# Kernel optimization log

Measured on AMD Instinct MI355X. Metric: run time of the kernel, lower is better.

The kernel has to match this reference:

```python
import jax, jax.numpy as jnp
import numpy as np

N_NODES = 100000
N_EDGES = 1600000
F_IN, F1, F2, F3 = 128, 128, 128, 64


def setup_inputs() -> dict:
    key = jax.random.key(0)
    ks = jax.random.split(key, 10)
    edge_index = jax.random.randint(ks[0], (2, N_EDGES), 0, N_NODES, dtype=jnp.int64)
    x = jax.random.normal(ks[1], (N_NODES, F_IN), dtype=jnp.float32)
    def glorot(k, fi, fo):
        s = (6.0 / (fi + fo)) ** 0.5
        return jax.random.uniform(k, (fi, fo), jnp.float32, -s, s)
    return {
        "edge_index": edge_index,
        "x": x,
        "W1": glorot(ks[2], F_IN, F1), "b1": jnp.zeros((F1,), jnp.float32),
        "W2": glorot(ks[3], F1, F2), "b2": jnp.zeros((F2,), jnp.float32),
        "W3": glorot(ks[4], F2, F3), "b3": jnp.zeros((F3,), jnp.float32),
        "W_att": glorot(ks[5], F3, F3),
    }


def _gcn_conv(x, W, b, src, dst, deg_inv_sqrt):
    h = x @ W  # [N, Fo]
    norm = deg_inv_sqrt[src] * deg_inv_sqrt[dst]  # [E]
    agg = jax.ops.segment_sum(h[src] * norm[:, None], dst, num_segments=x.shape[0])
    agg = agg + h * (deg_inv_sqrt * deg_inv_sqrt)[:, None]  # self-loop term
    return agg + b


def _attention_pool(emb, W_att):
    # SimGNN attention pooling
    ctx = jnp.tanh(jnp.mean(emb @ W_att, axis=0))          # [F3]
    scores = jax.nn.sigmoid(emb @ ctx)                      # [N]
    return emb.T @ scores[:, None]                          # [F3, 1]


def reference(edge_index, x, W1, b1, W2, b2, W3, b3, W_att):
    src, dst = edge_index[0], edge_index[1]
    n = x.shape[0]
    deg = jax.ops.segment_sum(jnp.ones_like(src, dtype=x.dtype), dst, num_segments=n) + 1.0
    dis = jax.lax.rsqrt(deg)
    h = jax.nn.relu(_gcn_conv(x, W1, b1, src, dst, dis))
    h = jax.nn.relu(_gcn_conv(h, W2, b2, src, dst, dis))
    h = _gcn_conv(h, W3, b3, src, dst, dis)                 # abstract_features [N, F3]
    pooled = _attention_pool(h, W_att)                      # [F3, 1]
    return h, pooled
```

## Files before the change

### kernel.cpp

```cpp
#include <hip/hip_runtime.h>
#include <hip/hip_bf16.h>

#define NN 100000
#define NE 1600000
#define NR 100032
#define NB2 196
#define NBLK 391
#define EPB 4096

#if defined(__has_builtin)
#  if __has_builtin(__builtin_amdgcn_cvt_pk_f32_fp8) && \
      __has_builtin(__builtin_amdgcn_cvt_pk_fp8_f32) && \
      __has_builtin(__builtin_amdgcn_cvt_f32_fp8)
#    define HWF8 1
#  endif
#endif

typedef float f32x2 __attribute__((ext_vector_type(2)));
typedef float f32x4 __attribute__((ext_vector_type(4)));
typedef short bf16x8 __attribute__((ext_vector_type(8)));

static __device__ __forceinline__ float bf2f(__hip_bfloat16 v) { return __bfloat162float(v); }
static __device__ __forceinline__ float bfu(unsigned short w) {
    return __uint_as_float((unsigned)w << 16);
}

static __device__ __forceinline__ float f8d_sw(unsigned b) {
    unsigned e = (b >> 3) & 15u, m = b & 7u;
    float mag;
    if (e == 0) mag = (float)m * 0.001953125f;
    else        mag = __uint_as_float(((e + 120u) << 23) | (m << 20));
    return (b & 0x80u) ? -mag : mag;
}
static __device__ __forceinline__ unsigned char f8e_sw(float x) {
    unsigned u = __float_as_uint(x);
    unsigned s = (u >> 31) << 7;
    unsigned au = u & 0x7fffffffu;
    if (au >= 0x43E00000u) return (unsigned char)(s | 0x7Eu);
    if (au <  0x3A800000u) return (unsigned char)s;
    if (au <  0x3C800000u) {
        float a = __uint_as_float(au);
        int m = (int)rintf(a * 512.0f);
        if (m >= 8) return (unsigned char)(s | 0x08u);
        return (unsigned char)(s | (unsigned)m);
    }
    au += 0x80000u;
    if (au >= 0x43E00000u) return (unsigned char)(s | 0x7Eu);
    unsigned e = (au >> 23) - 120u;
    unsigned m = (au >> 20) & 7u;
    return (unsigned char)(s | (e << 3) | m);
}

static __device__ __forceinline__ float f8d1(unsigned b) {
#ifdef HWF8
    return __builtin_amdgcn_cvt_f32_fp8((int)b, 0);
#else
    return f8d_sw(b);
#endif
}
static __device__ __forceinline__ void f8d2(unsigned short v, float& x0, float& x1) {
#ifdef HWF8
    f32x2 r = __builtin_amdgcn_cvt_pk_f32_fp8((int)(unsigned)v, false);
    x0 = r.x; x1 = r.y;
#else
    x0 = f8d_sw(v & 255u); x1 = f8d_sw(v >> 8);
#endif
}
static __device__ __forceinline__ void f8d4(unsigned u, float* o) {
#ifdef HWF8
    f32x2 lo = __builtin_amdgcn_cvt_pk_f32_fp8((int)u, false);
    f32x2 hi = __builtin_amdgcn_cvt_pk_f32_fp8((int)u, true);
    o[0] = lo.x; o[1] = lo.y; o[2] = hi.x; o[3] = hi.y;
#else
    o[0] = f8d_sw(u & 255u); o[1] = f8d_sw((u >> 8) & 255u);
    o[2] = f8d_sw((u >> 16) & 255u); o[3] = f8d_sw(u >> 24);
#endif
}
static __device__ __forceinline__ unsigned short f8e2(float a, float b) {
#ifdef HWF8
    float ca = fminf(fmaxf(a, -448.0f), 448.0f);
    float cb = fminf(fmaxf(b, -448.0f), 448.0f);
    int p = __builtin_amdgcn_cvt_pk_fp8_f32(ca, cb, 0, false);
    return (unsigned short)(p & 0xFFFF);
#else
    return (unsigned short)f8e_sw(a) | ((unsigned short)f8e_sw(b) << 8);
#endif
}
static __device__ __forceinline__ unsigned char f8e1(float a) {
    return (unsigned char)(f8e2(a, 0.0f) & 0xFF);
}
static __device__ __forceinline__ unsigned bfpack(float lo, float hi) {
    return (__float_as_uint(lo) >> 16) | (__float_as_uint(hi) & 0xFFFF0000u);
}

static __device__ __forceinline__ void acc8_add(f32x2* acc, uint2 v) {
#ifdef HWF8
    acc[0] += __builtin_amdgcn_cvt_pk_f32_fp8((int)v.x, false);
    acc[1] += __builtin_amdgcn_cvt_pk_f32_fp8((int)v.x, true);
    acc[2] += __builtin_amdgcn_cvt_pk_f32_fp8((int)v.y, false);
    acc[3] += __builtin_amdgcn_cvt_pk_f32_fp8((int)v.y, true);
#else
    unsigned u[2] = {v.x, v.y};
#pragma unroll
    for (int q = 0; q < 2; q++) {
        float o[4]; f8d4(u[q], o);
        acc[2 * q]     += (f32x2){o[0], o[1]};
        acc[2 * q + 1] += (f32x2){o[2], o[3]};
    }
#endif
}

__global__ void k_probe1(const unsigned short* __restrict__ xw,
                         const int* __restrict__ ei, int* __restrict__ raw) {
    int i = blockIdx.x * 256 + threadIdx.x;
    int nan = ((xw[i] & 0x7F80u) == 0x7F80u) ? 1 : 0;
    int odd = (ei[2 * i + 1] != 0) ? 1 : 0;
    unsigned long long bn = __ballot(nan);
    unsigned long long bo = __ballot(odd);
    if ((threadIdx.x & 63) == 0) {
        if (bn) atomicAdd(&raw[0], __popcll(bn));
        if (bo) atomicAdd(&raw[1], __popcll(bo));
    }
}
__global__ void k_probe2(const int* __restrict__ raw, int* __restrict__ flags) {
    if (threadIdx.x == 0) {
        flags[0] = (raw[0] > 0) ? 1 : 0;
        flags[1] = (raw[1] == 0) ? 1 : 0;
    }
}

static __device__ __forceinline__ int e_src(const int* ei, int e, int f64) {
    int v = f64 ? ei[2 * e] : ei[e];
    return min(max(v, 0), NN - 1);
}
static __device__ __forceinline__ int e_dst(const int* ei, int e, int f64) {
    int v = f64 ? ei[2 * (NE + e)] : ei[NE + e];
    return min(max(v, 0), NN - 1);
}
static __device__ __forceinline__ float ldx(const void* p, long long i, int f32) {
    return f32 ? ((const float*)p)[i] : bf2f(((const __hip_bfloat16*)p)[i]);
}

__global__ void cvt_params(const void* W1, const void* b1, const void* W2, const void* b2,
                           const void* W3, const void* b3, const void* Wa,
                           unsigned short* W1b, unsigned short* W2b, unsigned short* W3b,
                           float* b1f, float* b2f, float* b3f, float* Waf,
                           const int* flags) {
    int i = blockIdx.x * blockDim.x + threadIdx.x;
    int f = flags[0];
    if (i < 16384) {
        int j = i & 7, l = (i >> 3) & 63, c = (i >> 9) & 7, kc = i >> 12;
        int k = kc * 32 + ((l >> 4)) * 8 + j;
        int col = c * 16 + (l & 15);
        W1b[i] = __bfloat16_as_ushort(__float2bfloat16(ldx(W1, k * 128 + col, f)));
        W2b[i] = __bfloat16_as_ushort(__float2bfloat16(ldx(W2, k * 128 + col, f)));
    }
    if (i < 8192) {
        int j = i & 7, l = (i >> 3) & 63, c = (i >> 9) & 3, kc = i >> 11;
        int k = kc * 32 + ((l >> 4)) * 8 + j;
        int col = c * 16 + (l & 15);
        W3b[i] = __bfloat16_as_ushort(__float2bfloat16(ldx(W3, k * 64 + col, f)));
    }
    if (i < 4096)  Waf[i] = ldx(Wa, i, f);
    if (i < 128)   { b1f[i] = ldx(b1, i, f); b2f[i] = ldx(b2, i, f); }
    if (i < 64)    b3f[i] = ldx(b3, i, f);
}

__global__ void k_cvtx(const void* __restrict__ x, unsigned char* __restrict__ P,
                       const int* __restrict__ flags) {
    int i = blockIdx.x * blockDim.x + threadIdx.x;
    if (i >= (NN * 128) / 4) return;
    unsigned pk;
    if (flags[0]) {
        float4 v = ((const float4*)x)[i];
        pk = (unsigned)f8e2(v.x, v.y) | ((unsigned)f8e2(v.z, v.w) << 16);
    } else {
        ushort4 v = ((const ushort4*)x)[i];
        pk = (unsigned)f8e2(bfu(v.x), bfu(v.y)) | ((unsigned)f8e2(bfu(v.z), bfu(v.w)) << 16);
    }
    ((unsigned*)P)[i] = pk;
}

__global__ __launch_bounds__(256) void k_hist(const int* __restrict__ ei,
                                              int* __restrict__ ghist,
                                              const int* __restrict__ flags) {
    __shared__ int h[NB2];
    int blk = blockIdx.x, t = threadIdx.x;
    for (int i = t; i < NB2; i += 256) h[i] = 0;
    __syncthreads();
    int f64 = flags[1];
    int e0 = blk * EPB;
    for (int i = t; i < EPB; i += 256) {
        int e = e0 + i;
        if (e < NE) atomicAdd(&h[e_dst(ei, e, f64) >> 9], 1);
    }
    __syncthreads();
    for (int i = t; i < NB2; i += 256) ghist[blk * NB2 + i] = h[i];
}

__global__ __launch_bounds__(256) void k_off(const int* __restrict__ ghist,
                                             int* __restrict__ cbase,
                                             int* __restrict__ offm,
                                             int* __restrict__ rowptr) {
    __shared__ int tot[NB2];
    int t = threadIdx.x;
    if (t < NB2) {
        int s = 0;
        for (int blk = 0; blk < NBLK; blk++) s += ghist[blk * NB2 + t];
        tot[t] = s;
    }
    __syncthreads();
    if (t == 0) {
        int run = 0;
        for (int b = 0; b < NB2; b++) { cbase[b] = run; run += tot[b]; }
        cbase[NB2] = run;
        rowptr[NN] = run;
    }
    __syncthreads();
    if (t < NB2) {
        int run = cbase[t];
        for (int blk = 0; blk < NBLK; blk++) {
            offm[blk * NB2 + t] = run;
            run += ghist[blk * NB2 + t];
        }
    }
}

__global__ __launch_bounds__(256) void k_scatter(const int* __restrict__ ei,
                                                 const int* __restrict__ offm,
                                                 int* __restrict__ scratch,
                                                 const int* __restrict__ flags) {
    __shared__ int cur[NB2];
    int blk = blockIdx.x, t = threadIdx.x;
    for (int i = t; i < NB2; i += 256) cur[i] = offm[blk * NB2 + i];
    __syncthreads();
    int f64 = flags[1];
    int e0 = blk * EPB;
    for (int i = t; i < EPB; i += 256) {
        int e = e0 + i;
        if (e < NE) {
            int d = e_dst(ei, e, f64);
            int s = e_src(ei, e, f64);
            int p = atomicAdd(&cur[d >> 9], 1);
            p = min(max(p, 0), NE - 1);
            scratch[p] = s | ((d & 511) << 17);
        }
    }
}

__global__ __launch_bounds__(256) void k_build(const int* __restrict__ scratch,
                                               const int* __restrict__ cbase,
                                               int* __restrict__ rowptr,
                                               float* __restrict__ dis,
                                               int* __restrict__ csr) {
    __shared__ int hist[512];
    __shared__ int base[512];
    __shared__ int sd[256];
    int b = blockIdx.x, t = threadIdx.x;
    int n0 = b << 9;
    int s0 = cbase[b], s1 = cbase[b + 1];
    hist[t] = 0; hist[t + 256] = 0;
    __syncthreads();
    for (int i = s0 + t; i < s1; i += 256) {
        int dlo = (scratch[i] >> 17) & 511;
        atomicAdd(&hist[dlo], 1);
    }
    __syncthreads();
    int v0 = hist[2 * t], v1 = hist[2 * t + 1];
    int s = v0 + v1;
    sd[t] = s; __syncthreads();
    for (int o = 1; o < 256; o <<= 1) {
        int add = (t >= o) ? sd[t - o] : 0;
        __syncthreads();
        sd[t] += add;
        __syncthreads();
    }
    int run = s0 + sd[t] - s;
    base[2 * t] = run;
    base[2 * t + 1] = run + v0;
    int n = n0 + 2 * t;
    if (n < NN) {
        rowptr[n] = run;
        dis[n] = rsqrtf((float)v0 + 1.0f);
    }
    if (n + 1 < NN) {
        rowptr[n + 1] = run + v0;
        dis[n + 1] = rsqrtf((float)v1 + 1.0f);
    }
    __syncthreads();
    for (int i = s0 + t; i < s1; i += 256) {
        int v = scratch[i];
        int dlo = (v >> 17) & 511;
        int p = atomicAdd(&base[dlo], 1);
        p = min(max(p, 0), NE - 1);
        csr[p] = v & 0x1FFFF;
    }
}

template <int NCT>
__global__ __launch_bounds__(256) void k_xf_mfma(const unsigned char* __restrict__ A,
                                                 const unsigned short* __restrict__ Wf,
                                                 const float* __restrict__ dis,
                                                 unsigned char* __restrict__ O) {
    __shared__ unsigned short wl[NCT * 4 * 64 * 8];
    int t = threadIdx.x;
    int n0 = blockIdx.x * 64;
    {
        const uint4* wg = (const uint4*)Wf;
        uint4* wld = (uint4*)wl;
#pragma unroll
        for (int i = 0; i < NCT; i++) wld[i * 256 + t] = wg[i * 256 + t];
    }
    __syncthreads();
    int w = t >> 6, l = t & 63;
    int quad = l >> 4, m = l & 15;
    int arow = n0 + w * 16 + m;
    const unsigned char* ap = A + (size_t)arow * 128 + quad * 8;
    f32x4 acc[NCT];
#pragma unroll
    for (int c = 0; c < NCT; c++) acc[c] = (f32x4){0.0f, 0.0f, 0.0f, 0.0f};
#pragma unroll
    for (int kc = 0; kc < 4; kc++) {
        uint2 g = *(const uint2*)(ap + kc * 32);
        float o[8];
        f8d4(g.x, o); f8d4(g.y, o + 4);
        union { unsigned u[4]; bf16x8 v; } fr;
        fr.u[0] = bfpack(o[0], o[1]);
        fr.u[1] = bfpack(o[2], o[3]);
        fr.u[2] = bfpack(o[4], o[5]);
        fr.u[3] = bfpack(o[6], o[7]);
#pragma unroll
        for (int c = 0; c < NCT; c++) {
            bf16x8 bw = *(const bf16x8*)&wl[((kc * NCT + c) * 64 + l) * 8];
            acc[c] = __builtin_amdgcn_mfma_f32_16x16x32_bf16(fr.v, bw, acc[c], 0, 0, 0);
        }
    }
    int orow0 = n0 + w * 16 + quad * 4;
    float dsc[4];
#pragma unroll
    for (int r = 0; r < 4; r++) {
        int row = orow0 + r;
        dsc[r] = (row < NN) ? dis[row] : 0.0f;
    }
#pragma unroll
    for (int c = 0; c < NCT; c++) {
        int col = c * 16 + m;
#pragma unroll
        for (int r = 0; r < 4; r++) {
            int row = orow0 + r;
            if (row <= NN) O[(size_t)row * (NCT * 16) + col] = f8e1(acc[c][r] * dsc[r]);
        }
    }
}

template <bool RELU>
__global__ __launch_bounds__(256) void k_agg128(const unsigned char* __restrict__ Tb,
                                                const int* __restrict__ rowptr,
                                                const int* __restrict__ csr,
                                                const float* __restrict__ dis,
                                                const float* __restrict__ bias,
                                                unsigned char* __restrict__ H) {
    int n = blockIdx.x * 4 + (threadIdx.x >> 6);
    int lane = threadIdx.x & 63;
    int r = lane >> 4;
    int f = lane & 15;
    int fo = f << 3;
    float dn = dis[n];
    int s0 = rowptr[n], s1 = rowptr[n + 1];
    s0 = min(max(s0, 0), NE); s1 = min(max(s1, s0), NE);
    f32x2 acc[4];
#pragma unroll
    for (int k = 0; k < 4; k++) acc[k] = (f32x2){0.0f, 0.0f};
    if (r == 0) {
        uint2 v = *(const uint2*)(Tb + (((unsigned)n << 7) + (unsigned)fo));
        acc8_add(acc, v);
    }
    for (int base = s0; base < s1; base += 64) {
        int m = min(64, s1 - base);
        unsigned voff = (unsigned)NN << 7;
        if (lane < m) voff = (unsigned)csr[base + lane] << 7;
        int nq = (m + 15) >> 4;
        for (int q = 0; q < nq; q++) {
            int a0 = q * 64 + r * 4;
            unsigned vo0 = (unsigned)__builtin_amdgcn_ds_bpermute(a0,      (int)voff);
            unsigned vo1 = (unsigned)__builtin_amdgcn_ds_bpermute(a0 + 16, (int)voff);
            unsigned vo2 = (unsigned)__builtin_amdgcn_ds_bpermute(a0 + 32, (int)voff);
            unsigned vo3 = (unsigned)__builtin_amdgcn_ds_bpermute(a0 + 48, (int)voff);
            uint2 v0 = *(const uint2*)(Tb + (vo0 + (unsigned)fo));
            uint2 v1 = *(const uint2*)(Tb + (vo1 + (unsigned)fo));
            uint2 v2 = *(const uint2*)(Tb + (vo2 + (unsigned)fo));
            uint2 v3 = *(const uint2*)(Tb + (vo3 + (unsigned)fo));
            acc8_add(acc, v0);
            acc8_add(acc, v1);
            acc8_add(acc, v2);
            acc8_add(acc, v3);
        }
    }
#pragma unroll
    for (int k = 0; k < 4; k++) {
        acc[k].x += __shfl_xor(acc[k].x, 16, 64);
        acc[k].y += __shfl_xor(acc[k].y, 16, 64);
        acc[k].x += __shfl_xor(acc[k].x, 32, 64);
        acc[k].y += __shfl_xor(acc[k].y, 32, 64);
    }
    if (r == 0) {
        float4 bA = *(const float4*)(bias + fo);
        float4 bB = *(const float4*)(bias + fo + 4);
        float t[8];
        t[0] = acc[0].x * dn + bA.x; t[1] = acc[0].y * dn + bA.y;
        t[2] = acc[1].x * dn + bA.z; t[3] = acc[1].y * dn + bA.w;
        t[4] = acc[2].x * dn + bB.x; t[5] = acc[2].y * dn + bB.y;
        t[6] = acc[3].x * dn + bB.z; t[7] = acc[3].y * dn + bB.w;
        if (RELU) {
#pragma unroll
            for (int k = 0; k < 8; k++) t[k] = fmaxf(t[k], 0.0f);
        }
        unsigned lo = (unsigned)f8e2(t[0], t[1]) | ((unsigned)f8e2(t[2], t[3]) << 16);
        unsigned hi = (unsigned)f8e2(t[4], t[5]) | ((unsigned)f8e2(t[6], t[7]) << 16);
        *(uint2*)(H + (((size_t)n << 7) + (size_t)fo)) = make_uint2(lo, hi);
    }
}

__global__ __launch_bounds__(256) void k_agg64(const unsigned char* __restrict__ Tb,
                                               const int* __restrict__ rowptr,
                                               const int* __restrict__ csr,
                                               const float* __restrict__ dis,
                                               const float* __restrict__ bias,
                                               unsigned short* __restrict__ Hb) {
    int lane = threadIdx.x & 63;
    int half = lane >> 5;
    int hl = lane & 31;
    int n = blockIdx.x * 8 + (threadIdx.x >> 6) * 2 + half;
    int r = hl >> 3;
    int f = hl & 7;
    int fo = f << 3;
    float dn = dis[n];
    int s0 = rowptr[n], s1 = rowptr[n + 1];
    s0 = min(max(s0, 0), NE); s1 = min(max(s1, s0), NE);
    f32x2 acc[4];
#pragma unroll
    for (int k = 0; k < 4; k++) acc[k] = (f32x2){0.0f, 0.0f};
    if (r == 0) {
        uint2 v = *(const uint2*)(Tb + (((unsigned)n << 6) + (unsigned)fo));
        acc8_add(acc, v);
    }
    int ab = half << 7;
    for (int base = s0; base < s1; base += 32) {
        int m = min(32, s1 - base);
        unsigned voff = (unsigned)NN << 6;
        if (hl < m) voff = (unsigned)csr[base + hl] << 6;
        int nq = (m + 15) >> 4;
        for (int q = 0; q < nq; q++) {
            int a0 = ab + q * 64 + r * 4;
            unsigned vo0 = (unsigned)__builtin_amdgcn_ds_bpermute(a0,      (int)voff);
            unsigned vo1 = (unsigned)__builtin_amdgcn_ds_bpermute(a0 + 16, (int)voff);
            unsigned vo2 = (unsigned)__builtin_amdgcn_ds_bpermute(a0 + 32, (int)voff);
            unsigned vo3 = (unsigned)__builtin_amdgcn_ds_bpermute(a0 + 48, (int)voff);
            uint2 v0 = *(const uint2*)(Tb + (vo0 + (unsigned)fo));
            uint2 v1 = *(const uint2*)(Tb + (vo1 + (unsigned)fo));
            uint2 v2 = *(const uint2*)(Tb + (vo2 + (unsigned)fo));
            uint2 v3 = *(const uint2*)(Tb + (vo3 + (unsigned)fo));
            acc8_add(acc, v0);
            acc8_add(acc, v1);
            acc8_add(acc, v2);
            acc8_add(acc, v3);
        }
    }
#pragma unroll
    for (int k = 0; k < 4; k++) {
        acc[k].x += __shfl_xor(acc[k].x, 8, 64);
        acc[k].y += __shfl_xor(acc[k].y, 8, 64);
        acc[k].x += __shfl_xor(acc[k].x, 16, 64);
        acc[k].y += __shfl_xor(acc[k].y, 16, 64);
    }
    if (r == 0) {
        float4 bA = *(const float4*)(bias + fo);
        float4 bB = *(const float4*)(bias + fo + 4);
        float t[8];
        t[0] = acc[0].x * dn + bA.x; t[1] = acc[0].y * dn + bA.y;
        t[2] = acc[1].x * dn + bA.z; t[3] = acc[1].y * dn + bA.w;
        t[4] = acc[2].x * dn + bB.x; t[5] = acc[2].y * dn + bB.y;
        t[6] = acc[3].x * dn + bB.z; t[7] = acc[3].y * dn + bB.w;
        unsigned p0 = (unsigned)__bfloat16_as_ushort(__float2bfloat16(t[0])) |
                      ((unsigned)__bfloat16_as_ushort(__float2bfloat16(t[1])) << 16);
        unsigned p1 = (unsigned)__bfloat16_as_ushort(__float2bfloat16(t[2])) |
                      ((unsigned)__bfloat16_as_ushort(__float2bfloat16(t[3])) << 16);
        unsigned p2 = (unsigned)__bfloat16_as_ushort(__float2bfloat16(t[4])) |
                      ((unsigned)__bfloat16_as_ushort(__float2bfloat16(t[5])) << 16);
        unsigned p3 = (unsigned)__bfloat16_as_ushort(__float2bfloat16(t[6])) |
                      ((unsigned)__bfloat16_as_ushort(__float2bfloat16(t[7])) << 16);
        *(uint4*)(Hb + (((size_t)n << 6) + (size_t)fo)) = make_uint4(p0, p1, p2, p3);
    }
}

__global__ __launch_bounds__(512) void k_colsum(const unsigned short* __restrict__ h3,
                                                float* __restrict__ colsum) {
    int t = threadIdx.x;
    int lane = t & 63;
    int rg = lane >> 4, cq = lane & 15;
    int wid = (blockIdx.x * 512 + t) >> 6;
    int nw = (gridDim.x * 512) >> 6;
    float a0 = 0, a1 = 0, a2 = 0, a3 = 0;
    for (int r = wid * 4 + rg; r < NN; r += nw * 4) {
        uint2 v = *(const uint2*)(h3 + ((size_t)r << 6) + cq * 4);
        a0 += bfu((unsigned short)(v.x & 0xFFFF));
        a1 += bfu((unsigned short)(v.x >> 16));
        a2 += bfu((unsigned short)(v.y & 0xFFFF));
        a3 += bfu((unsigned short)(v.y >> 16));
    }
    a0 += __shfl_xor(a0, 16, 64); a0 += __shfl_xor(a0, 32, 64);
    a1 += __shfl_xor(a1, 16, 64); a1 += __shfl_xor(a1, 32, 64);
    a2 += __shfl_xor(a2, 16, 64); a2 += __shfl_xor(a2, 32, 64);
    a3 += __shfl_xor(a3, 16, 64); a3 += __shfl_xor(a3, 32, 64);
    __shared__ float part[8][64];
    int w = t >> 6;
    if (rg == 0) {
        part[w][cq * 4 + 0] = a0;
        part[w][cq * 4 + 1] = a1;
        part[w][cq * 4 + 2] = a2;
        part[w][cq * 4 + 3] = a3;
    }
    __syncthreads();
    if (t < 64) {
        float s = 0;
#pragma unroll
        for (int i = 0; i < 8; i++) s += part[i][t];
        atomicAdd(&colsum[t], s);
    }
}

__global__ void k_ctx(const float* __restrict__ colsum, const float* __restrict__ Wa,
                      float* __restrict__ ctx) {
    __shared__ float ms[64];
    int j = threadIdx.x;
    ms[j] = colsum[j] * (1.0f / NN);
    __syncthreads();
    float s = 0.0f;
#pragma unroll
    for (int k = 0; k < 64; k++) s += ms[k] * Wa[k * 64 + j];
    ctx[j] = tanhf(s);
}

__global__ __launch_bounds__(512) void k_pool(const unsigned short* __restrict__ h3,
                                              const float* __restrict__ ctx,
                                              float* __restrict__ pooled) {
    int t = threadIdx.x;
    int lane = t & 63;
    int rg = lane >> 4, cq = lane & 15;
    int wid = (blockIdx.x * 512 + t) >> 6;
    int nw = (gridDim.x * 512) >> 6;
    float c0 = ctx[cq * 4 + 0], c1 = ctx[cq * 4 + 1];
    float c2 = ctx[cq * 4 + 2], c3 = ctx[cq * 4 + 3];
    float q0 = 0, q1 = 0, q2 = 0, q3 = 0;
    for (int r = wid * 4 + rg; r < NN; r += nw * 4) {
        uint2 v = *(const uint2*)(h3 + ((size_t)r << 6) + cq * 4);
        float x0 = bfu((unsigned short)(v.x & 0xFFFF));
        float x1 = bfu((unsigned short)(v.x >> 16));
        float x2 = bfu((unsigned short)(v.y & 0xFFFF));
        float x3 = bfu((unsigned short)(v.y >> 16));
        float p = x0 * c0 + x1 * c1 + x2 * c2 + x3 * c3;
        p += __shfl_xor(p, 1, 64);
        p += __shfl_xor(p, 2, 64);
        p += __shfl_xor(p, 4, 64);
        p += __shfl_xor(p, 8, 64);
        float sc = 1.0f / (1.0f + expf(-p));
        q0 += sc * x0; q1 += sc * x1; q2 += sc * x2; q3 += sc * x3;
    }
    q0 += __shfl_xor(q0, 16, 64); q0 += __shfl_xor(q0, 32, 64);
    q1 += __shfl_xor(q1, 16, 64); q1 += __shfl_xor(q1, 32, 64);
    q2 += __shfl_xor(q2, 16, 64); q2 += __shfl_xor(q2, 32, 64);
    q3 += __shfl_xor(q3, 16, 64); q3 += __shfl_xor(q3, 32, 64);
    __shared__ float part[8][64];
    int w = t >> 6;
    if (rg == 0) {
        part[w][cq * 4 + 0] = q0;
        part[w][cq * 4 + 1] = q1;
        part[w][cq * 4 + 2] = q2;
        part[w][cq * 4 + 3] = q3;
    }
    __syncthreads();
    if (t < 64) {
        float s = 0;
#pragma unroll
        for (int i = 0; i < 8; i++) s += part[i][t];
        atomicAdd(&pooled[t], s);
    }
}

__global__ void k_out(const unsigned short* __restrict__ h3, const float* __restrict__ pooled,
                      void* __restrict__ out, const int* __restrict__ flags) {
    int q = blockIdx.x * blockDim.x + threadIdx.x;
    if (q >= 1600016) return;
    long long i0 = (long long)q * 4;
    float v[4];
#pragma unroll
    for (int k = 0; k < 4; k++) {
        long long i = i0 + k;
        v[k] = (i < 6400000LL) ? bfu(h3[i]) : pooled[i - 6400000LL];
    }
    if (flags[0]) {
        *(float4*)((float*)out + i0) = make_float4(v[0], v[1], v[2], v[3]);
    } else {
        unsigned lo = (unsigned)__bfloat16_as_ushort(__float2bfloat16(v[0])) |
                      ((unsigned)__bfloat16_as_ushort(__float2bfloat16(v[1])) << 16);
        unsigned hi = (unsigned)__bfloat16_as_ushort(__float2bfloat16(v[2])) |
                      ((unsigned)__bfloat16_as_ushort(__float2bfloat16(v[3])) << 16);
        *(uint2*)((unsigned short*)out + i0) = make_uint2(lo, hi);
    }
}

static constexpr size_t AL(size_t x) { return (x + 255) & ~size_t(255); }
static constexpr size_t OFF_FLAGS  = 0;
static constexpr size_t OFF_RAW    = OFF_FLAGS + 256;
static constexpr size_t OFF_GHIST  = OFF_RAW + 256;
static constexpr size_t OFF_OFFM   = OFF_GHIST + AL((size_t)NBLK * NB2 * 4);
static constexpr size_t OFF_CBASE  = OFF_OFFM + AL((size_t)NBLK * NB2 * 4);
static constexpr size_t OFF_ROWPTR = OFF_CBASE + AL((NB2 + 1) * 4);
static constexpr size_t OFF_CSR    = OFF_ROWPTR + AL((NN + 1) * 4);
static constexpr size_t OFF_DIS    = OFF_CSR + AL((size_t)NE * 4);
static constexpr size_t OFF_P      = OFF_DIS + AL(NN * 4);
static constexpr size_t OFF_W1B    = OFF_P + AL((size_t)NR * 128);
static constexpr size_t OFF_W2B    = OFF_W1B + AL(16384 * 2);
static constexpr size_t OFF_W3B    = OFF_W2B + AL(16384 * 2);
static constexpr size_t OFF_B1F    = OFF_W3B + AL(8192 * 2);
static constexpr size_t OFF_B2F    = OFF_B1F + AL(128 * 4);
static constexpr size_t OFF_B3F    = OFF_B2F + AL(128 * 4);
static constexpr size_t OFF_WAF    = OFF_B3F + AL(64 * 4);
static constexpr size_t OFF_COLSUM = OFF_WAF + AL(4096 * 4);
static constexpr size_t OFF_POOLED = OFF_COLSUM + AL(64 * 4);
static constexpr size_t OFF_CTX    = OFF_POOLED + AL(64 * 4);

extern "C" void kernel_launch(void* const* d_in, const int* in_sizes, int n_in,
                              void* d_out, int out_size, void* d_ws, size_t ws_size,
                              hipStream_t stream) {
    const int* ei = (const int*)d_in[0];
    const void* x  = d_in[1];
    const void* W1 = d_in[2];
    const void* b1 = d_in[3];
    const void* W2 = d_in[4];
    const void* b2 = d_in[5];
    const void* W3 = d_in[6];
    const void* b3 = d_in[7];
    const void* Wa = d_in[8];

    char* ws = (char*)d_ws;
    int*   flags  = (int*)(ws + OFF_FLAGS);
    int*   raw    = (int*)(ws + OFF_RAW);
    int*   ghist  = (int*)(ws + OFF_GHIST);
    int*   offm   = (int*)(ws + OFF_OFFM);
    int*   cbase  = (int*)(ws + OFF_CBASE);
    int*   rowptr = (int*)(ws + OFF_ROWPTR);
    int*   csr    = (int*)(ws + OFF_CSR);
    float* dis    = (float*)(ws + OFF_DIS);
    unsigned char*  P    = (unsigned char*)(ws + OFF_P);
    int*            scrA = (int*)(ws + OFF_P);
    unsigned short* Hb   = (unsigned short*)(ws + OFF_P);
    unsigned short* W1b = (unsigned short*)(ws + OFF_W1B);
    unsigned short* W2b = (unsigned short*)(ws + OFF_W2B);
    unsigned short* W3b = (unsigned short*)(ws + OFF_W3B);
    float* b1f    = (float*)(ws + OFF_B1F);
    float* b2f    = (float*)(ws + OFF_B2F);
    float* b3f    = (float*)(ws + OFF_B3F);
    float* Waf    = (float*)(ws + OFF_WAF);
    float* colsum = (float*)(ws + OFF_COLSUM);
    float* pooled = (float*)(ws + OFF_POOLED);
    float* ctx    = (float*)(ws + OFF_CTX);

    unsigned char* Q = (unsigned char*)d_out;

    hipMemsetAsync(raw, 0, 256, stream);
    hipMemsetAsync(colsum, 0, 64 * 4, stream);
    hipMemsetAsync(pooled, 0, 64 * 4, stream);

    k_probe1<<<256, 256, 0, stream>>>((const unsigned short*)x, ei, raw);
    k_probe2<<<1, 64, 0, stream>>>(raw, flags);
    cvt_params<<<64, 256, 0, stream>>>(W1, b1, W2, b2, W3, b3, Wa,
                                       W1b, W2b, W3b, b1f, b2f, b3f, Waf, flags);

    k_hist<<<NBLK, 256, 0, stream>>>(ei, ghist, flags);
    k_off<<<1, 256, 0, stream>>>(ghist, cbase, offm, rowptr);
    k_scatter<<<NBLK, 256, 0, stream>>>(ei, offm, scrA, flags);
    k_build<<<NB2, 256, 0, stream>>>(scrA, cbase, rowptr, dis, csr);

    k_cvtx<<<(NN * 128 / 4 + 255) / 256, 256, 0, stream>>>(x, P, flags);

    k_xf_mfma<8><<<NR / 64, 256, 0, stream>>>(P, W1b, dis, Q);
    k_agg128<true><<<NN / 4, 256, 0, stream>>>(Q, rowptr, csr, dis, b1f, P);
    k_xf_mfma<8><<<NR / 64, 256, 0, stream>>>(P, W2b, dis, Q);
    k_agg128<true><<<NN / 4, 256, 0, stream>>>(Q, rowptr, csr, dis, b2f, P);
    k_xf_mfma<4><<<NR / 64, 256, 0, stream>>>(P, W3b, dis, Q);
    k_agg64<<<NN / 8, 256, 0, stream>>>(Q, rowptr, csr, dis, b3f, Hb);

    k_colsum<<<256, 512, 0, stream>>>(Hb, colsum);
    k_ctx<<<1, 64, 0, stream>>>(colsum, Waf, ctx);
    k_pool<<<256, 512, 0, stream>>>(Hb, ctx, pooled);

    k_out<<<(1600016 + 255) / 256, 256, 0, stream>>>(Hb, pooled, d_out, flags);
}
```

Measured before the change: 415.2 us.

## Fuse prep kernels, write output inside pooling, vectorize MFMA epilogue stores

Merges the flag probe, parameter conversion and x-to-fp8 conversion into one prep kernel that reads raw counters directly, removing several small launches and memsets. The ctx computation moves into the tail of k_colsum using a last-block atomic counter. The final output copy is folded into k_pool, so the separate full-size pass over H3 goes away and only the pooled vector is written by a tiny tail kernel. In the MFMA transform the operand order is swapped so each lane holds four consecutive columns, which allows packed 32-bit fp8 stores instead of byte stores. The cost is a more complex grid-level sync in colsum and reliance on the raw counters being read correctly in every kernel.

```diff
diff --git a/kernel.cpp b/kernel.cpp
--- a/kernel.cpp
+++ b/kernel.cpp
@@ -51,21 +51,6 @@
     return (unsigned char)(s | (e << 3) | m);
 }
 
-static __device__ __forceinline__ float f8d1(unsigned b) {
-#ifdef HWF8
-    return __builtin_amdgcn_cvt_f32_fp8((int)b, 0);
-#else
-    return f8d_sw(b);
-#endif
-}
-static __device__ __forceinline__ void f8d2(unsigned short v, float& x0, float& x1) {
-#ifdef HWF8
-    f32x2 r = __builtin_amdgcn_cvt_pk_f32_fp8((int)(unsigned)v, false);
-    x0 = r.x; x1 = r.y;
-#else
-    x0 = f8d_sw(v & 255u); x1 = f8d_sw(v >> 8);
-#endif
-}
 static __device__ __forceinline__ void f8d4(unsigned u, float* o) {
 #ifdef HWF8
     f32x2 lo = __builtin_amdgcn_cvt_pk_f32_fp8((int)u, false);
@@ -85,9 +70,6 @@
 #else
     return (unsigned short)f8e_sw(a) | ((unsigned short)f8e_sw(b) << 8);
 #endif
-}
-static __device__ __forceinline__ unsigned char f8e1(float a) {
-    return (unsigned char)(f8e2(a, 0.0f) & 0xFF);
 }
 static __device__ __forceinline__ unsigned bfpack(float lo, float hi) {
     return (__float_as_uint(lo) >> 16) | (__float_as_uint(hi) & 0xFFFF0000u);
@@ -122,12 +104,6 @@
         if (bo) atomicAdd(&raw[1], __popcll(bo));
     }
 }
-__global__ void k_probe2(const int* __restrict__ raw, int* __restrict__ flags) {
-    if (threadIdx.x == 0) {
-        flags[0] = (raw[0] > 0) ? 1 : 0;
-        flags[1] = (raw[1] == 0) ? 1 : 0;
-    }
-}
 
 static __device__ __forceinline__ int e_src(const int* ei, int e, int f64) {
     int v = f64 ? ei[2 * e] : ei[e];
@@ -141,14 +117,36 @@
     return f32 ? ((const float*)p)[i] : bf2f(((const __hip_bfloat16*)p)[i]);
 }
 
-__global__ void cvt_params(const void* W1, const void* b1, const void* W2, const void* b2,
-                           const void* W3, const void* b3, const void* Wa,
-                           unsigned short* W1b, unsigned short* W2b, unsigned short* W3b,
-                           float* b1f, float* b2f, float* b3f, float* Waf,
-                           const int* flags) {
-    int i = blockIdx.x * blockDim.x + threadIdx.x;
-    int f = flags[0];
-    if (i < 16384) {
+__global__ __launch_bounds__(256) void k_prep(const void* __restrict__ x,
+                                              const void* W1, const void* b1,
+                                              const void* W2, const void* b2,
+                                              const void* W3, const void* b3,
+                                              const void* Wa,
+                                              unsigned short* W1b, unsigned short* W2b,
+                                              unsigned short* W3b,
+                                              float* b1f, float* b2f, float* b3f,
+                                              float* Waf,
+                                              unsigned char* __restrict__ P,
+                                              const int* __restrict__ raw,
+                                              float* colsum, float* pooled, int* wsync) {
+    int t = threadIdx.x;
+    int gi = blockIdx.x;
+    int f = raw[0] > 0;
+    if (gi < 12500) {
+        int i = gi * 256 + t;
+        unsigned pk;
+        if (f) {
+            float4 v = ((const float4*)x)[i];
+            pk = (unsigned)f8e2(v.x, v.y) | ((unsigned)f8e2(v.z, v.w) << 16);
+        } else {
+            ushort4 v = ((const ushort4*)x)[i];
+            pk = (unsigned)f8e2(bfu(v.x), bfu(v.y)) | ((unsigned)f8e2(bfu(v.z), bfu(v.w)) << 16);
+        }
+        ((unsigned*)P)[i] = pk;
+        return;
+    }
+    int i = (gi - 12500) * 256 + t;
+    {
         int j = i & 7, l = (i >> 3) & 63, c = (i >> 9) & 7, kc = i >> 12;
         int k = kc * 32 + ((l >> 4)) * 8 + j;
         int col = c * 16 + (l & 15);
@@ -164,31 +162,24 @@
     if (i < 4096)  Waf[i] = ldx(Wa, i, f);
     if (i < 128)   { b1f[i] = ldx(b1, i, f); b2f[i] = ldx(b2, i, f); }
     if (i < 64)    b3f[i] = ldx(b3, i, f);
-}
-
-__global__ void k_cvtx(const void* __restrict__ x, unsigned char* __restrict__ P,
-                       const int* __restrict__ flags) {
-    int i = blockIdx.x * blockDim.x + threadIdx.x;
-    if (i >= (NN * 128) / 4) return;
-    unsigned pk;
-    if (flags[0]) {
-        float4 v = ((const float4*)x)[i];
-        pk = (unsigned)f8e2(v.x, v.y) | ((unsigned)f8e2(v.z, v.w) << 16);
-    } else {
-        ushort4 v = ((const ushort4*)x)[i];
-        pk = (unsigned)f8e2(bfu(v.x), bfu(v.y)) | ((unsigned)f8e2(bfu(v.z), bfu(v.w)) << 16);
-    }
-    ((unsigned*)P)[i] = pk;
+    if (gi == 12500) {
+        if (t < 64) { colsum[t] = 0.0f; pooled[t] = 0.0f; }
+        if (t == 0) *wsync = 0;
+    }
+    if (gi == 12501) {
+        for (int z = t; z < (NR - NN) * 32; z += 256)
+            ((unsigned*)(P + (size_t)NN * 128))[z] = 0u;
+    }
 }
 
 __global__ __launch_bounds__(256) void k_hist(const int* __restrict__ ei,
                                               int* __restrict__ ghist,
-                                              const int* __restrict__ flags) {
+                                              const int* __restrict__ raw) {
     __shared__ int h[NB2];
     int blk = blockIdx.x, t = threadIdx.x;
     for (int i = t; i < NB2; i += 256) h[i] = 0;
     __syncthreads();
-    int f64 = flags[1];
+    int f64 = (raw[1] == 0);
     int e0 = blk * EPB;
     for (int i = t; i < EPB; i += 256) {
         int e = e0 + i;
@@ -229,12 +220,12 @@
 __global__ __launch_bounds__(256) void k_scatter(const int* __restrict__ ei,
                                                  const int* __restrict__ offm,
                                                  int* __restrict__ scratch,
-                                                 const int* __restrict__ flags) {
+                                                 const int* __restrict__ raw) {
     __shared__ int cur[NB2];
     int blk = blockIdx.x, t = threadIdx.x;
     for (int i = t; i < NB2; i += 256) cur[i] = offm[blk * NB2 + i];
     __syncthreads();
-    int f64 = flags[1];
+    int f64 = (raw[1] == 0);
     int e0 = blk * EPB;
     for (int i = t; i < EPB; i += 256) {
         int e = e0 + i;
@@ -314,8 +305,8 @@
     __syncthreads();
     int w = t >> 6, l = t & 63;
     int quad = l >> 4, m = l & 15;
-    int arow = n0 + w * 16 + m;
-    const unsigned char* ap = A + (size_t)arow * 128 + quad * 8;
+    int node = n0 + w * 16 + m;
+    const unsigned char* ap = A + (size_t)node * 128 + quad * 8;
     f32x4 acc[NCT];
 #pragma unroll
     for (int c = 0; c < NCT; c++) acc[c] = (f32x4){0.0f, 0.0f, 0.0f, 0.0f};
@@ -332,23 +323,17 @@
 #pragma unroll
         for (int c = 0; c < NCT; c++) {
             bf16x8 bw = *(const bf16x8*)&wl[((kc * NCT + c) * 64 + l) * 8];
-            acc[c] = __builtin_amdgcn_mfma_f32_16x16x32_bf16(fr.v, bw, acc[c], 0, 0, 0);
-        }
-    }
-    int orow0 = n0 + w * 16 + quad * 4;
-    float dsc[4];
-#pragma unroll
-    for (int r = 0; r < 4; r++) {
-        int row = orow0 + r;
-        dsc[r] = (row < NN) ? dis[row] : 0.0f;
-    }
-#pragma unroll
-    for (int c = 0; c < NCT; c++) {
-        int col = c * 16 + m;
-#pragma unroll
-        for (int r = 0; r < 4; r++) {
-            int row = orow0 + r;
-            if (row <= NN) O[(size_t)row * (NCT * 16) + col] = f8e1(acc[c][r] * dsc[r]);
+            acc[c] = __builtin_amdgcn_mfma_f32_16x16x32_bf16(bw, fr.v, acc[c], 0, 0, 0);
+        }
+    }
+    float d = (node < NN) ? dis[node] : 0.0f;
+    if (node <= NN) {
+        unsigned char* orow = O + (size_t)node * (NCT * 16) + quad * 4;
+#pragma unroll
+        for (int c = 0; c < NCT; c++) {
+            unsigned pk = (unsigned)f8e2(acc[c][0] * d, acc[c][1] * d)
+                        | ((unsigned)f8e2(acc[c][2] * d, acc[c][3] * d) << 16);
+            *(unsigned*)(orow + c * 16) = pk;
         }
     }
 }
@@ -494,7 +479,10 @@
 }
 
 __global__ __launch_bounds__(512) void k_colsum(const unsigned short* __restrict__ h3,
-                                                float* __restrict__ colsum) {
+                                                float* __restrict__ colsum,
+                                                const float* __restrict__ Waf,
+                                                float* __restrict__ ctx,
+                                                int* __restrict__ wsync) {
     int t = threadIdx.x;
     int lane = t & 63;
     int rg = lane >> 4, cq = lane & 15;
@@ -527,28 +515,41 @@
         for (int i = 0; i < 8; i++) s += part[i][t];
         atomicAdd(&colsum[t], s);
     }
-}
-
-__global__ void k_ctx(const float* __restrict__ colsum, const float* __restrict__ Wa,
-                      float* __restrict__ ctx) {
-    __shared__ float ms[64];
-    int j = threadIdx.x;
-    ms[j] = colsum[j] * (1.0f / NN);
-    __syncthreads();
-    float s = 0.0f;
-#pragma unroll
-    for (int k = 0; k < 64; k++) s += ms[k] * Wa[k * 64 + j];
-    ctx[j] = tanhf(s);
+    __shared__ int lastf;
+    __syncthreads();
+    if (t == 0) {
+        __threadfence();
+        int old = atomicAdd(wsync, 1);
+        lastf = (old == (int)gridDim.x - 1) ? 1 : 0;
+    }
+    __syncthreads();
+    if (lastf) {
+        __shared__ float ms[64];
+        if (t < 64) {
+            __threadfence();
+            ms[t] = atomicAdd(&colsum[t], 0.0f) * (1.0f / NN);
+        }
+        __syncthreads();
+        if (t < 64) {
+            float s = 0.0f;
+#pragma unroll
+            for (int k = 0; k < 64; k++) s += ms[k] * Waf[k * 64 + t];
+            ctx[t] = tanhf(s);
+        }
+    }
 }
 
 __global__ __launch_bounds__(512) void k_pool(const unsigned short* __restrict__ h3,
                                               const float* __restrict__ ctx,
-                                              float* __restrict__ pooled) {
+                                              float* __restrict__ pooled,
+                                              void* __restrict__ out,
+                                              const int* __restrict__ raw) {
     int t = threadIdx.x;
     int lane = t & 63;
     int rg = lane >> 4, cq = lane & 15;
     int wid = (blockIdx.x * 512 + t) >> 6;
     int nw = (gridDim.x * 512) >> 6;
+    int f32o = raw[0] > 0;
     float c0 = ctx[cq * 4 + 0], c1 = ctx[cq * 4 + 1];
     float c2 = ctx[cq * 4 + 2], c3 = ctx[cq * 4 + 3];
     float q0 = 0, q1 = 0, q2 = 0, q3 = 0;
@@ -558,6 +559,12 @@
         float x1 = bfu((unsigned short)(v.x >> 16));
         float x2 = bfu((unsigned short)(v.y & 0xFFFF));
         float x3 = bfu((unsigned short)(v.y >> 16));
+        if (f32o) {
+            *(float4*)((float*)out + ((size_t)r << 6) + cq * 4) =
+                make_float4(x0, x1, x2, x3);
+        } else {
+            *(uint2*)((unsigned short*)out + ((size_t)r << 6) + cq * 4) = v;
+        }
         float p = x0 * c0 + x1 * c1 + x2 * c2 + x3 * c3;
         p += __shfl_xor(p, 1, 64);
         p += __shfl_xor(p, 2, 64);
@@ -587,25 +594,14 @@
     }
 }
 
-__global__ void k_out(const unsigned short* __restrict__ h3, const float* __restrict__ pooled,
-                      void* __restrict__ out, const int* __restrict__ flags) {
-    int q = blockIdx.x * blockDim.x + threadIdx.x;
-    if (q >= 1600016) return;
-    long long i0 = (long long)q * 4;
-    float v[4];
-#pragma unroll
-    for (int k = 0; k < 4; k++) {
-        long long i = i0 + k;
-        v[k] = (i < 6400000LL) ? bfu(h3[i]) : pooled[i - 6400000LL];
-    }
-    if (flags[0]) {
-        *(float4*)((float*)out + i0) = make_float4(v[0], v[1], v[2], v[3]);
+__global__ void k_tail(const float* __restrict__ pooled, void* __restrict__ out,
+                       const int* __restrict__ raw) {
+    int j = threadIdx.x;
+    if (raw[0] > 0) {
+        ((float*)out)[6400000 + j] = pooled[j];
     } else {
-        unsigned lo = (unsigned)__bfloat16_as_ushort(__float2bfloat16(v[0])) |
-                      ((unsigned)__bfloat16_as_ushort(__float2bfloat16(v[1])) << 16);
-        unsigned hi = (unsigned)__bfloat16_as_ushort(__float2bfloat16(v[2])) |
-                      ((unsigned)__bfloat16_as_ushort(__float2bfloat16(v[3])) << 16);
-        *(uint2*)((unsigned short*)out + i0) = make_uint2(lo, hi);
+        ((unsigned short*)out)[6400000 + j] =
+            __bfloat16_as_ushort(__float2bfloat16(pooled[j]));
     }
 }
 
@@ -629,6 +625,7 @@
 static constexpr size_t OFF_COLSUM = OFF_WAF + AL(4096 * 4);
 static constexpr size_t OFF_POOLED = OFF_COLSUM + AL(64 * 4);
 static constexpr size_t OFF_CTX    = OFF_POOLED + AL(64 * 4);
+static constexpr size_t OFF_SYNC   = OFF_CTX + AL(64 * 4);
 
 extern "C" void kernel_launch(void* const* d_in, const int* in_sizes, int n_in,
                               void* d_out, int out_size, void* d_ws, size_t ws_size,
@@ -644,7 +641,6 @@
     const void* Wa = d_in[8];
 
     char* ws = (char*)d_ws;
-    int*   flags  = (int*)(ws + OFF_FLAGS);
     int*   raw    = (int*)(ws + OFF_RAW);
     int*   ghist  = (int*)(ws + OFF_GHIST);
     int*   offm   = (int*)(ws + OFF_OFFM);
@@ -665,24 +661,22 @@
     float* colsum = (float*)(ws + OFF_COLSUM);
     float* pooled = (float*)(ws + OFF_POOLED);
     float* ctx    = (float*)(ws + OFF_CTX);
+    int*   wsync  = (int*)(ws + OFF_SYNC);
 
     unsigned char* Q = (unsigned char*)d_out;
 
     hipMemsetAsync(raw, 0, 256, stream);
-    hipMemsetAsync(colsum, 0, 64 * 4, stream);
-    hipMemsetAsync(pooled, 0, 64 * 4, stream);
 
     k_probe1<<<256, 256, 0, stream>>>((const unsigned short*)x, ei, raw);
-    k_probe2<<<1, 64, 0, stream>>>(raw, flags);
-    cvt_params<<<64, 256, 0, stream>>>(W1, b1, W2, b2, W3, b3, Wa,
-                                       W1b, W2b, W3b, b1f, b2f, b3f, Waf, flags);
-
-    k_hist<<<NBLK, 256, 0, stream>>>(ei, ghist, flags);
+
+    k_hist<<<NBLK, 256, 0, stream>>>(ei, ghist, raw);
     k_off<<<1, 256, 0, stream>>>(ghist, cbase, offm, rowptr);
-    k_scatter<<<NBLK, 256, 0, stream>>>(ei, offm, scrA, flags);
+    k_scatter<<<NBLK, 256, 0, stream>>>(ei, offm, scrA, raw);
     k_build<<<NB2, 256, 0, stream>>>(scrA, cbase, rowptr, dis, csr);
 
-    k_cvtx<<<(NN * 128 / 4 + 255) / 256, 256, 0, stream>>>(x, P, flags);
+    k_prep<<<12564, 256, 0, stream>>>(x, W1, b1, W2, b2, W3, b3, Wa,
+                                      W1b, W2b, W3b, b1f, b2f, b3f, Waf,
+                                      P, raw, colsum, pooled, wsync);
 
     k_xf_mfma<8><<<NR / 64, 256, 0, stream>>>(P, W1b, dis, Q);
     k_agg128<true><<<NN / 4, 256, 0, stream>>>(Q, rowptr, csr, dis, b1f, P);
@@ -691,9 +685,7 @@
     k_xf_mfma<4><<<NR / 64, 256, 0, stream>>>(P, W3b, dis, Q);
     k_agg64<<<NN / 8, 256, 0, stream>>>(Q, rowptr, csr, dis, b3f, Hb);
 
-    k_colsum<<<256, 512, 0, stream>>>(Hb, colsum);
-    k_ctx<<<1, 64, 0, stream>>>(colsum, Waf, ctx);
-    k_pool<<<256, 512, 0, stream>>>(Hb, ctx, pooled);
-
-    k_out<<<(1600016 + 255) / 256, 256, 0, stream>>>(Hb, pooled, d_out, flags);
-}
+    k_colsum<<<256, 512, 0, stream>>>(Hb, colsum, Waf, ctx, wsync);
+    k_pool<<<256, 512, 0, stream>>>(Hb, ctx, pooled, d_out, raw);
+    k_tail<<<1, 64, 0, stream>>>(pooled, d_out, raw);
+}
```

Result: faster. 393.1 us (-5.3%).
